# Kernel tuning notes

Measured on AMD Instinct MI355X. Metric: run time of the kernel, lower is better.

The kernel has to match this reference:

```python
import jax, jax.numpy as jnp
import numpy as np

N, E, L, F, HID, OUT = 20000, 200000, 5, 4, 128, 3


def _lin(x, w, b):
    # torch Linear convention: w is [out, in]
    return x @ w.T + b


def setup_inputs() -> dict:
    key = jax.random.key(0)
    ks = iter(jax.random.split(key, 40))
    nrm = lambda shape, s=0.05: jax.random.normal(next(ks), shape, dtype=jnp.float32) * s
    inp = {
        'x': jax.random.normal(next(ks), (N, L, F), dtype=jnp.float32),
        'edge_index': jax.random.randint(next(ks), (2, E), 0, N, dtype=jnp.int64),
        'edge_attr': jax.random.normal(next(ks), (E, F), dtype=jnp.float32),
        'batch': jnp.zeros((N,), dtype=jnp.int64),
        'node_type': jax.random.normal(next(ks), (N, 1), dtype=jnp.float32),
        # PastStateEncoder params
        'emb': nrm((L, F), 1.0),
        'conv_w': nrm((HID, 2 * F, 3)),  # Conv1d(8,128,3) OIW
        'conv_b': nrm((HID,)),
        # FusionLayer Linear(129,128)
        'fuse_w': nrm((HID, HID + 1)), 'fuse_b': nrm((HID,)),
        # gnn1 EdgeModel: Linear(2*128+4,128), Linear(128,128)
        'g1e_w1': nrm((HID, 2 * HID + F)), 'g1e_b1': nrm((HID,)),
        'g1e_w2': nrm((HID, HID)), 'g1e_b2': nrm((HID,)),
        # gnn1 NodeModel: Linear(256,128), Linear(128,128)
        'g1n_w1': nrm((HID, 2 * HID)), 'g1n_b1': nrm((HID,)),
        'g1n_w2': nrm((HID, HID)), 'g1n_b2': nrm((HID,)),
        # gnn2 EdgeModel: Linear(2*128+128,128), Linear(128,128)
        'g2e_w1': nrm((HID, 3 * HID)), 'g2e_b1': nrm((HID,)),
        'g2e_w2': nrm((HID, HID)), 'g2e_b2': nrm((HID,)),
        # gnn2 NodeModel
        'g2n_w1': nrm((HID, 2 * HID)), 'g2n_b1': nrm((HID,)),
        'g2n_w2': nrm((HID, HID)), 'g2n_b2': nrm((HID,)),
        # final_mlp: Linear(128,128), BN(128), Linear(128,3)
        'fm_w1': nrm((HID, HID)), 'fm_b1': nrm((HID,)),
        'bn_g': jnp.ones((HID,), dtype=jnp.float32), 'bn_b': jnp.zeros((HID,), dtype=jnp.float32),
        'fm_w2': nrm((OUT, HID)), 'fm_b2': nrm((OUT,)),
    }
    return inp


def _encoder(x, emb, conv_w, conv_b):
    # x: [N, L, F]; append learned positional embedding -> [N, L, 2F]
    n = x.shape[0]
    xe = jnp.concatenate([x, jnp.broadcast_to(emb[None], (n, L, F))], axis=-1)
    xc = xe.transpose(0, 2, 1)  # [N, 2F, L]
    y = jax.lax.conv_general_dilated(
        xc, conv_w, window_strides=(1,), padding=[(1, 1)],
        dimension_numbers=('NCW', 'OIW', 'NCW'))
    y = y + conv_b[None, :, None]
    return y.mean(axis=-1)  # [N, HID]


def _edge_mlp(src, dst, ea, w1, b1, w2, b2):
    h = jax.nn.relu(_lin(jnp.concatenate([src, dst, ea], axis=1), w1, b1))
    return _lin(h, w2, b2)


def _node_mlp(x_row, ea, w1, b1, w2, b2):
    h = jax.nn.relu(_lin(jnp.concatenate([x_row, ea], axis=1), w1, b1))
    return _lin(h, w2, b2)


def reference(x, edge_index, edge_attr, batch, node_type,
              emb, conv_w, conv_b, fuse_w, fuse_b,
              g1e_w1, g1e_b1, g1e_w2, g1e_b2, g1n_w1, g1n_b1, g1n_w2, g1n_b2,
              g2e_w1, g2e_b1, g2e_w2, g2e_b2, g2n_w1, g2n_b1, g2n_w2, g2n_b2,
              fm_w1, fm_b1, bn_g, bn_b, fm_w2, fm_b2):
    row, col = edge_index[0], edge_index[1]
    h = _encoder(x, emb, conv_w, conv_b)                     # [N,128]
    h = _lin(jnp.concatenate([h, node_type], axis=-1), fuse_w, fuse_b)  # [N,128]
    # gnn1 (MetaLayer: edge model then node model; node model here is per-edge)
    ea = _edge_mlp(h[row], h[col], edge_attr, g1e_w1, g1e_b1, g1e_w2, g1e_b2)  # [E,128]
    h = _node_mlp(h[row], ea, g1n_w1, g1n_b1, g1n_w2, g1n_b2)                  # [E,128]
    # gnn2 (h now lives on edges; indices < N <= E remain valid, matching torch)
    ea = _edge_mlp(h[row], h[col], ea, g2e_w1, g2e_b1, g2e_w2, g2e_b2)
    h = _node_mlp(h[row], ea, g2n_w1, g2n_b1, g2n_w2, g2n_b2)
    # final head on edge_attr: Linear -> BatchNorm1d (training stats) -> ReLU -> Linear
    z = _lin(ea, fm_w1, fm_b1)
    mu = z.mean(axis=0)
    var = z.var(axis=0)  # biased, matches torch BN normalization
    z = (z - mu) * jax.lax.rsqrt(var + 1e-5) * bn_g + bn_b
    z = jax.nn.relu(z)
    return _lin(z, fm_w2, fm_b2)  # [E,3]
```

## Files before the change

### kernel.cpp

```cpp
#include <hip/hip_runtime.h>

#define N_NODES 20000
#define N_EDGES 200000
#define HID 128
#define STR 136
#define NBLK 3125
#define NREP 64

typedef unsigned short u16;
using bf16x8 = __attribute__((ext_vector_type(8))) __bf16;
using f32x4  = __attribute__((ext_vector_type(4))) float;

__device__ __forceinline__ u16 f2bf(float f) {
  union { float f; unsigned u; } v; v.f = f;
  unsigned u = v.u;
  return (u16)((u + 0x7FFFu + ((u >> 16) & 1u)) >> 16);
}
__device__ __forceinline__ float bf2f(unsigned s) {
  union { unsigned u; float f; } v; v.u = s << 16;
  return v.f;
}
__device__ __forceinline__ bf16x8 ld8(const u16* p) { return *(const bf16x8*)p; }

__device__ __forceinline__ void zero_acc8(f32x4 acc[4]) {
#pragma unroll
  for (int i = 0; i < 4; ++i) acc[i] = (f32x4){0.f, 0.f, 0.f, 0.f};
}

template <int KSTEPS, typename AF>
__device__ __forceinline__ void wgemm8(const u16* __restrict__ PW, AF afrag,
                                       f32x4 acc[4], int lane, int wave) {
  const u16* pb = PW + (wave * 64 + lane) * 8;
  bf16x8 b[2];
  b[0] = ld8(pb);
#pragma unroll
  for (int ks = 0; ks < KSTEPS; ++ks) {
    const int cur = ks & 1;
    if (ks + 1 < KSTEPS) b[cur ^ 1] = ld8(pb + (ks + 1) * 4096);
#pragma unroll
    for (int mt = 0; mt < 4; ++mt) {
      bf16x8 a = afrag(ks, mt);
      acc[mt] = __builtin_amdgcn_mfma_f32_16x16x32_bf16(a, b[cur], acc[mt], 0, 0, 0);
    }
  }
}

template <bool RELU>
__device__ __forceinline__ void epi_store8(u16* buf, const f32x4 acc[4],
                                           const float* __restrict__ bias,
                                           int lane, int wave) {
  const int c = lane & 15, q = lane >> 4;
  const float bb = bias[wave * 16 + c];
  const int col = wave * 16 + c;
#pragma unroll
  for (int mt = 0; mt < 4; ++mt)
#pragma unroll
    for (int r = 0; r < 4; ++r) {
      float v = acc[mt][r] + bb;
      if (RELU) v = fmaxf(v, 0.f);
      buf[(mt * 16 + q * 4 + r) * STR + col] = f2bf(v);
    }
}

__device__ __forceinline__ void flush_buf8(const u16* buf, u16* __restrict__ gout,
                                           int e0, int tid) {
#pragma unroll
  for (int it = 0; it < 2; ++it) {
    int cid = tid + it * 512, e = cid >> 4, p = cid & 15;
    uint4 v = *(const uint4*)(buf + e * STR + p * 8);
    *(uint4*)(gout + (size_t)(e0 + e) * HID + p * 8) = v;
  }
}

__device__ __forceinline__ void stage_gather8(const int* __restrict__ rowI,
                                              const int* __restrict__ colI,
                                              const u16* __restrict__ htab,
                                              u16* B0, u16* B1,
                                              int e0, int lane, int wave) {
  const int r = lane >> 4, p = lane & 15;
#pragma unroll
  for (int it = 0; it < 4; ++it) {
    int j = wave * 16 + it * 4 + r;
    int e = j & 63;
    int id = (j < 64) ? rowI[e0 + e] : colI[e0 + e];
    uint4 v = *(const uint4*)(htab + (size_t)id * HID + p * 8);
    *(uint4*)(((j < 64) ? B0 : B1) + e * STR + p * 8) = v;
  }
}

__global__ __launch_bounds__(128) void k_prep1(
    const float* __restrict__ emb, const float* __restrict__ conv_w,
    const float* __restrict__ conv_b, const float* __restrict__ fuse_w,
    const float* __restrict__ fuse_b,
    const float* __restrict__ fm_w1, const float* __restrict__ g2e_b2,
    const float* __restrict__ fm_b1, const float* __restrict__ w6,
    float* __restrict__ Mt, float* __restrict__ C0, float* __restrict__ Wnt,
    float* __restrict__ b67, float* __restrict__ W67, float* __restrict__ bnrep) {
  __shared__ float red[22][129];
  __shared__ float w7s[128];
  const int o = blockIdx.x;
  const int j = threadIdx.x;
  bnrep[o * 128 + j] = 0.f;
  float A[21];
  {
    float b0 = conv_b[j];
#pragma unroll
    for (int p = 0; p < 5; ++p) {
#pragma unroll
      for (int i = 0; i < 8; ++i) {
        float s = 0.f;
#pragma unroll
        for (int k = 0; k < 3; ++k) {
          int t = p + 1 - k;
          if (t >= 0 && t < 5) s += conv_w[(j * 8 + i) * 3 + k];
        }
        s *= 0.2f;
        if (i < 4) A[p * 4 + i] = s;
        else b0 += emb[p * 4 + (i - 4)] * s;
      }
    }
    A[20] = b0;
  }
  float w = fuse_w[o * 129 + j];
  float w7 = fm_w1[o * 128 + j];
  w7s[j] = w7;
#pragma unroll
  for (int qq = 0; qq < 21; ++qq) red[qq][j] = w * A[qq];
  red[21][j] = w7 * g2e_b2[j];
  __syncthreads();
  if (j < 22) {
    float s = 0.f;
    for (int t = 0; t < 128; ++t) s += red[j][t];
    if (j < 20)      Mt[j * 128 + o] = s;
    else if (j == 20) C0[o] = s + fuse_b[o];
    else              b67[o] = s + fm_b1[o];
  }
  if (j == 0) Wnt[o] = fuse_w[o * 129 + 128];
  float s = 0.f;
  for (int t = 0; t < 128; ++t) s += w7s[t] * w6[t * 128 + j];
  W67[o * 128 + j] = s;
}

struct PackArgs {
  const float* src[6];
  u16* dst[6];
  int Kin[6];
  int ksCum[7];
};

__global__ __launch_bounds__(256) void k_prep2(
    PackArgs pa, const float* __restrict__ x, const float* __restrict__ node_type,
    const float* __restrict__ Mt, const float* __restrict__ C0,
    const float* __restrict__ Wnt, u16* __restrict__ h2) {
  if (blockIdx.x < 41) {
    int bk = blockIdx.x;
    int mi = 0;
    while (bk >= pa.ksCum[mi + 1]) ++mi;
    int ks = bk - pa.ksCum[mi];
    const float* W = pa.src[mi];
    u16* D = pa.dst[mi] + ks * 4096;
    int Kin = pa.Kin[mi];
#pragma unroll
    for (int t = 0; t < 16; ++t) {
      int el = t * 256 + (int)threadIdx.x;
      int j = el & 7, ln = (el >> 3) & 63, ntile = el >> 9;
      int k = ks * 32 + ((ln >> 4) << 3) + j;
      int n = ntile * 16 + (ln & 15);
      float v = (k < Kin) ? W[n * Kin + k] : 0.0f;
      D[el] = f2bf(v);
    }
    return;
  }
  __shared__ float xs[16][20], nts[16], mts[20 * 128];
  const int tid = threadIdx.x;
  const int n0 = ((int)blockIdx.x - 41) * 16;
  for (int i = tid; i < 320; i += 256) xs[i / 20][i % 20] = x[n0 * 20 + i];
  if (tid < 16) nts[tid] = node_type[n0 + tid];
  for (int i = tid; i < 2560; i += 256) mts[i] = Mt[i];
  __syncthreads();
  const int nl = tid >> 4;
  const int c0 = (tid & 15) * 8;
  float nt = nts[nl];
  union { u16 s[8]; uint4 u; } o;
#pragma unroll
  for (int i = 0; i < 8; ++i) {
    int ch = c0 + i;
    float acc = C0[ch] + Wnt[ch] * nt;
#pragma unroll
    for (int qq = 0; qq < 20; ++qq) acc += xs[nl][qq] * mts[qq * 128 + ch];
    o.s[i] = f2bf(acc);
  }
  *(uint4*)(h2 + (size_t)(n0 + nl) * HID + c0) = o.u;
}

__global__ __launch_bounds__(512, 8) void k_gnn1(
    const int* __restrict__ eidx, const float* __restrict__ eattr,
    const u16* __restrict__ h2, const u16* __restrict__ pW1, const u16* __restrict__ pW2,
    const u16* __restrict__ pW3, const u16* __restrict__ pW4, const float* __restrict__ b1,
    const float* __restrict__ b2, const float* __restrict__ b3, const float* __restrict__ b4,
    u16* __restrict__ ea1, u16* __restrict__ h3) {
  __shared__ __align__(16) u16 B0[64 * STR], B1[64 * STR];
  const int tid = threadIdx.x, lane = tid & 63, wave = tid >> 6;
  const int e0 = blockIdx.x * 64;
  const int m = lane & 15, q = lane >> 4;
  const int aoff = m * STR + q * 8;
  const int* rowI = eidx;
  const int* colI = eidx + N_EDGES;

  stage_gather8(rowI, colI, h2, B0, B1, e0, lane, wave);

  bf16x8 ef[4];
#pragma unroll
  for (int mt = 0; mt < 4; ++mt) {
    union { u16 s[8]; uint4 u; bf16x8 v; } t;
    t.u = make_uint4(0u, 0u, 0u, 0u);
    if (q == 0) {
      float4 a = *(const float4*)(eattr + (size_t)(e0 + mt * 16 + m) * 4);
      t.s[0] = f2bf(a.x); t.s[1] = f2bf(a.y); t.s[2] = f2bf(a.z); t.s[3] = f2bf(a.w);
    }
    ef[mt] = t.v;
  }
  __syncthreads();

  f32x4 acc[4];
  zero_acc8(acc);
  wgemm8<9>(pW1, [&](int ks, int mt) -> bf16x8 {
    if (ks < 4) return ld8(B0 + aoff + mt * 16 * STR + ks * 32);
    if (ks < 8) return ld8(B1 + aoff + mt * 16 * STR + (ks - 4) * 32);
    return ef[mt];
  }, acc, lane, wave);
  __syncthreads();
  epi_store8<true>(B1, acc, b1, lane, wave);
  __syncthreads();

  zero_acc8(acc);
  wgemm8<4>(pW2, [&](int ks, int mt) -> bf16x8 {
    return ld8(B1 + aoff + mt * 16 * STR + ks * 32);
  }, acc, lane, wave);
  epi_store8<false>(B0, acc, b2, lane, wave);
  __syncthreads();
  flush_buf8(B0, ea1, e0, tid);

  if (e0 < N_NODES) {
#pragma unroll
    for (int it = 0; it < 2; ++it) {
      int e = wave * 8 + it * 4 + q;
      int id = rowI[e0 + e];
      uint4 v = *(const uint4*)(h2 + (size_t)id * HID + m * 8);
      *(uint4*)(B1 + e * STR + m * 8) = v;
    }
    __syncthreads();

    zero_acc8(acc);
    wgemm8<8>(pW3, [&](int ks, int mt) -> bf16x8 {
      if (ks < 4) return ld8(B1 + aoff + mt * 16 * STR + ks * 32);
      return ld8(B0 + aoff + mt * 16 * STR + (ks - 4) * 32);
    }, acc, lane, wave);
    __syncthreads();
    epi_store8<true>(B1, acc, b3, lane, wave);
    __syncthreads();

    zero_acc8(acc);
    wgemm8<4>(pW4, [&](int ks, int mt) -> bf16x8 {
      return ld8(B1 + aoff + mt * 16 * STR + ks * 32);
    }, acc, lane, wave);
    epi_store8<false>(B0, acc, b4, lane, wave);
    __syncthreads();
    flush_buf8(B0, h3, e0, tid);
  }
}

__global__ __launch_bounds__(512, 8) void k_gnn2(
    const int* __restrict__ eidx, const u16* __restrict__ h3, u16* ea1z,
    const u16* __restrict__ pW5, const u16* __restrict__ pW67,
    const float* __restrict__ b5, const float* __restrict__ b67,
    float* __restrict__ bnrep) {
  __shared__ __align__(16) u16 B0[64 * STR], B1[64 * STR];
  const int tid = threadIdx.x, lane = tid & 63, wave = tid >> 6;
  const int e0 = blockIdx.x * 64;
  const int m = lane & 15, q = lane >> 4;
  const int aoff = m * STR + q * 8;
  const int* rowI = eidx;
  const int* colI = eidx + N_EDGES;

  stage_gather8(rowI, colI, h3, B0, B1, e0, lane, wave);
  __syncthreads();

  f32x4 acc[4];
  zero_acc8(acc);
  wgemm8<8>(pW5, [&](int ks, int mt) -> bf16x8 {
    if (ks < 4) return ld8(B0 + aoff + mt * 16 * STR + ks * 32);
    return ld8(B1 + aoff + mt * 16 * STR + (ks - 4) * 32);
  }, acc, lane, wave);
  __syncthreads();

#pragma unroll
  for (int it = 0; it < 2; ++it) {
    int cid = tid + it * 512, e = cid >> 4, p = cid & 15;
    uint4 v = *(const uint4*)(ea1z + (size_t)(e0 + e) * HID + p * 8);
    *(uint4*)(B0 + e * STR + p * 8) = v;
  }
  __syncthreads();

  wgemm8<4>(pW5 + 8 * 4096, [&](int ks, int mt) -> bf16x8 {
    return ld8(B0 + aoff + mt * 16 * STR + ks * 32);
  }, acc, lane, wave);
  epi_store8<true>(B1, acc, b5, lane, wave);
  __syncthreads();

  zero_acc8(acc);
  wgemm8<4>(pW67, [&](int ks, int mt) -> bf16x8 {
    return ld8(B1 + aoff + mt * 16 * STR + ks * 32);
  }, acc, lane, wave);

  {
    const int c = lane & 15;
    const int col = wave * 16 + c;
    const float bb = b67[col];
    float s0 = 0.f, q0 = 0.f;
#pragma unroll
    for (int mt = 0; mt < 4; ++mt)
#pragma unroll
      for (int r = 0; r < 4; ++r) {
        float v0 = acc[mt][r] + bb;
        s0 += v0; q0 += v0 * v0;
        int row = mt * 16 + q * 4 + r;
        B0[row * STR + col] = f2bf(v0);
      }
    s0 += __shfl_xor(s0, 16); s0 += __shfl_xor(s0, 32);
    q0 += __shfl_xor(q0, 16); q0 += __shfl_xor(q0, 32);
    if (lane < 16) {
      float* slot = bnrep + ((int)blockIdx.x & (NREP - 1)) * 256;
      atomicAdd(&slot[wave * 16 + lane], s0);
      atomicAdd(&slot[128 + wave * 16 + lane], q0);
    }
  }
  __syncthreads();
  flush_buf8(B0, ea1z, e0, tid);
}

__global__ __launch_bounds__(256) void k_head(const u16* __restrict__ z,
                                              const float* __restrict__ bnrep,
                                              const float* __restrict__ bn_g,
                                              const float* __restrict__ bn_b,
                                              const float* __restrict__ w2,
                                              const float* __restrict__ b2,
                                              float* __restrict__ out) {
  __shared__ float sh_s[128], sh_h[128], sh_w0[128], sh_w1[128], sh_w2[128];
  const int tid = threadIdx.x;
  {
    float s = 0.f;
    for (int r = 0; r < NREP; ++r) s += bnrep[r * 256 + tid];
    __shared__ float acc2[256];
    acc2[tid] = s;
    __syncthreads();
    if (tid < 128) {
      const float inv = 1.0f / (float)N_EDGES;
      float mu = acc2[tid] * inv;
      float var = acc2[128 + tid] * inv - mu * mu;
      float sc = bn_g[tid] * rsqrtf(var + 1e-5f);
      sh_s[tid] = sc;
      sh_h[tid] = bn_b[tid] - mu * sc;
      sh_w0[tid] = w2[tid];
      sh_w1[tid] = w2[128 + tid];
      sh_w2[tid] = w2[256 + tid];
    }
    __syncthreads();
  }
  const int lane = tid & 63, wave = tid >> 6;
  const int g = lane >> 4;
  const int p = lane & 15;
  const int c0 = p * 8;
  const float bb0 = b2[0], bb1 = b2[1], bb2 = b2[2];
#pragma unroll 4
  for (int it = 0; it < 16; ++it) {
    int e = (int)blockIdx.x * 256 + wave * 64 + it * 4 + g;
    if (e >= N_EDGES) break;
    uint4 v = *(const uint4*)(z + (size_t)e * HID + c0);
    unsigned wv[4] = {v.x, v.y, v.z, v.w};
    float a0 = 0.f, a1 = 0.f, a2 = 0.f;
#pragma unroll
    for (int k = 0; k < 4; ++k) {
      int ch = c0 + k * 2;
      float lo = bf2f(wv[k] & 0xffffu), hi = bf2f(wv[k] >> 16);
      float r0 = fmaxf(fmaf(lo, sh_s[ch], sh_h[ch]), 0.f);
      float r1 = fmaxf(fmaf(hi, sh_s[ch + 1], sh_h[ch + 1]), 0.f);
      a0 += r0 * sh_w0[ch] + r1 * sh_w0[ch + 1];
      a1 += r0 * sh_w1[ch] + r1 * sh_w1[ch + 1];
      a2 += r0 * sh_w2[ch] + r1 * sh_w2[ch + 1];
    }
#pragma unroll
    for (int off = 1; off < 16; off <<= 1) {
      a0 += __shfl_xor(a0, off);
      a1 += __shfl_xor(a1, off);
      a2 += __shfl_xor(a2, off);
    }
    if (p < 3) out[e * 3 + p] = (p == 0) ? a0 + bb0 : (p == 1) ? a1 + bb1 : a2 + bb2;
  }
}

extern "C" void kernel_launch(void* const* d_in, const int* in_sizes, int n_in,
                              void* d_out, int out_size, void* d_ws, size_t ws_size,
                              hipStream_t stream) {
  const float* x         = (const float*)d_in[0];
  const int* eidx        = (const int*)d_in[1];
  const float* eattr     = (const float*)d_in[2];
  const float* node_type = (const float*)d_in[4];
  const float* emb       = (const float*)d_in[5];
  const float* conv_w    = (const float*)d_in[6];
  const float* conv_b    = (const float*)d_in[7];
  const float* fuse_w    = (const float*)d_in[8];
  const float* fuse_b    = (const float*)d_in[9];
  const float* g1e_w1    = (const float*)d_in[10];
  const float* g1e_b1    = (const float*)d_in[11];
  const float* g1e_w2    = (const float*)d_in[12];
  const float* g1e_b2    = (const float*)d_in[13];
  const float* g1n_w1    = (const float*)d_in[14];
  const float* g1n_b1    = (const float*)d_in[15];
  const float* g1n_w2    = (const float*)d_in[16];
  const float* g1n_b2    = (const float*)d_in[17];
  const float* g2e_w1    = (const float*)d_in[18];
  const float* g2e_b1    = (const float*)d_in[19];
  const float* g2e_w2    = (const float*)d_in[20];
  const float* g2e_b2    = (const float*)d_in[21];
  const float* fm_w1     = (const float*)d_in[26];
  const float* fm_b1     = (const float*)d_in[27];
  const float* bn_g      = (const float*)d_in[28];
  const float* bn_b      = (const float*)d_in[29];
  const float* fm_w2     = (const float*)d_in[30];
  const float* fm_b2     = (const float*)d_in[31];
  float* out = (float*)d_out;

  char* ws = (char*)d_ws;
  size_t off = 0;
  auto take = [&](size_t bytes) {
    void* p = ws + off;
    off = (off + bytes + 255) & ~(size_t)255;
    return p;
  };
  u16* h2   = (u16*)take((size_t)N_NODES * HID * 2);
  u16* h3   = (u16*)take((size_t)20032 * HID * 2);
  u16* ea1z = (u16*)take((size_t)N_EDGES * HID * 2);
  float* Mt    = (float*)take(20 * 128 * 4);
  float* C0    = (float*)take(128 * 4);
  float* Wnt   = (float*)take(128 * 4);
  float* b67   = (float*)take(128 * 4);
  float* W67f  = (float*)take(128 * 128 * 4);
  float* bnrep = (float*)take((size_t)NREP * 256 * 4);
  u16* pW1  = (u16*)take(9 * 4096 * 2);
  u16* pW2  = (u16*)take(4 * 4096 * 2);
  u16* pW3  = (u16*)take(8 * 4096 * 2);
  u16* pW4  = (u16*)take(4 * 4096 * 2);
  u16* pW5  = (u16*)take(12 * 4096 * 2);
  u16* pW67 = (u16*)take(4 * 4096 * 2);

  k_prep1<<<128, 128, 0, stream>>>(emb, conv_w, conv_b, fuse_w, fuse_b,
                                   fm_w1, g2e_b2, fm_b1, g2e_w2,
                                   Mt, C0, Wnt, b67, W67f, bnrep);

  PackArgs pa;
  const float* srcs[6] = {g1e_w1, g1e_w2, g1n_w1, g1n_w2, g2e_w1, W67f};
  u16* dsts[6] = {pW1, pW2, pW3, pW4, pW5, pW67};
  int kins[6] = {260, 128, 256, 128, 384, 128};
  int kst[6] = {9, 4, 8, 4, 12, 4};
  int cum = 0;
  for (int i = 0; i < 6; ++i) {
    pa.src[i] = srcs[i]; pa.dst[i] = dsts[i]; pa.Kin[i] = kins[i];
    pa.ksCum[i] = cum; cum += kst[i];
  }
  pa.ksCum[6] = cum;

  k_prep2<<<41 + N_NODES / 16, 256, 0, stream>>>(pa, x, node_type, Mt, C0, Wnt, h2);
  k_gnn1<<<NBLK, 512, 0, stream>>>(eidx, eattr, h2, pW1, pW2, pW3, pW4,
                                   g1e_b1, g1e_b2, g1n_b1, g1n_b2, ea1z, h3);
  k_gnn2<<<NBLK, 512, 0, stream>>>(eidx, h3, ea1z, pW5, pW67,
                                   g2e_b1, b67, bnrep);
  k_head<<<(N_EDGES + 255) / 256, 256, 0, stream>>>(ea1z, bnrep, bn_g, bn_b,
                                                    fm_w2, fm_b2, out);
}
```

Baseline: 232.4 us.

## Fuse all stages into one cooperative persistent kernel with grid syncs

Replaces the five separate launches with a single cooperative kernel that runs prep, encode, two GNN stages and the head, separated by grid-wide syncs. Edge tiles are claimed dynamically through an atomic counter in a persistent loop. The goal is to remove launch gaps and tail effects between kernels. The cost is grid.sync overhead, lower occupancy (512 blocks, launch bounds of 4 per CU), and atomic contention on the tile counter. A multi-kernel fallback runs if the cooperative launch fails.

```diff
diff --git a/kernel.cpp b/kernel.cpp
--- a/kernel.cpp
+++ b/kernel.cpp
@@ -1,4 +1,7 @@
 #include <hip/hip_runtime.h>
+#include <hip/hip_cooperative_groups.h>
+
+namespace cg = cooperative_groups;
 
 #define N_NODES 20000
 #define N_EDGES 200000
@@ -88,207 +91,213 @@
   }
 }
 
-__global__ __launch_bounds__(128) void k_prep1(
-    const float* __restrict__ emb, const float* __restrict__ conv_w,
-    const float* __restrict__ conv_b, const float* __restrict__ fuse_w,
-    const float* __restrict__ fuse_b,
-    const float* __restrict__ fm_w1, const float* __restrict__ g2e_b2,
-    const float* __restrict__ fm_b1, const float* __restrict__ w6,
-    float* __restrict__ Mt, float* __restrict__ C0, float* __restrict__ Wnt,
-    float* __restrict__ b67, float* __restrict__ W67, float* __restrict__ bnrep) {
-  __shared__ float red[22][129];
-  __shared__ float w7s[128];
-  const int o = blockIdx.x;
-  const int j = threadIdx.x;
-  bnrep[o * 128 + j] = 0.f;
-  float A[21];
-  {
-    float b0 = conv_b[j];
-#pragma unroll
-    for (int p = 0; p < 5; ++p) {
-#pragma unroll
-      for (int i = 0; i < 8; ++i) {
-        float s = 0.f;
-#pragma unroll
-        for (int k = 0; k < 3; ++k) {
-          int t = p + 1 - k;
-          if (t >= 0 && t < 5) s += conv_w[(j * 8 + i) * 3 + k];
+struct FusedArgs {
+  const float *x, *eattr, *node_type, *emb, *conv_w, *conv_b, *fuse_w, *fuse_b;
+  const float *g1e_b1, *g1e_b2, *g1n_b1, *g1n_b2, *g2e_b1, *g2e_b2;
+  const float *fm_w1, *fm_b1, *bn_g, *bn_b, *fm_w2, *fm_b2, *w6;
+  const int* eidx;
+  float* out;
+  u16 *h2, *h3, *ea1z, *pW1, *pW2, *pW3, *pW4, *pW5, *pW67;
+  float *Mt, *C0, *Wnt, *b67, *W67f, *bnrep;
+  int* ctr;
+  const float* psrc[6];
+  u16* pdst[6];
+  int pKin[6];
+  int pCum[7];
+};
+
+
+__device__ __forceinline__ void phase_prep1(const FusedArgs& fa, int bid, int gdim,
+                                            int tid, u16* SM) {
+  float* red = (float*)SM;
+  float* w7s = red + 22 * 129;
+  for (int o = bid; o < 128; o += gdim) {
+    __syncthreads();
+    if (tid < 128) {
+      const int j = tid;
+      float A[21];
+      {
+        float b0 = fa.conv_b[j];
+#pragma unroll
+        for (int p = 0; p < 5; ++p) {
+#pragma unroll
+          for (int i = 0; i < 8; ++i) {
+            float s = 0.f;
+#pragma unroll
+            for (int k = 0; k < 3; ++k) {
+              int tt = p + 1 - k;
+              if (tt >= 0 && tt < 5) s += fa.conv_w[(j * 8 + i) * 3 + k];
+            }
+            s *= 0.2f;
+            if (i < 4) A[p * 4 + i] = s;
+            else b0 += fa.emb[p * 4 + (i - 4)] * s;
+          }
         }
-        s *= 0.2f;
-        if (i < 4) A[p * 4 + i] = s;
-        else b0 += emb[p * 4 + (i - 4)] * s;
+        A[20] = b0;
       }
-    }
-    A[20] = b0;
-  }
-  float w = fuse_w[o * 129 + j];
-  float w7 = fm_w1[o * 128 + j];
-  w7s[j] = w7;
-#pragma unroll
-  for (int qq = 0; qq < 21; ++qq) red[qq][j] = w * A[qq];
-  red[21][j] = w7 * g2e_b2[j];
-  __syncthreads();
-  if (j < 22) {
-    float s = 0.f;
-    for (int t = 0; t < 128; ++t) s += red[j][t];
-    if (j < 20)      Mt[j * 128 + o] = s;
-    else if (j == 20) C0[o] = s + fuse_b[o];
-    else              b67[o] = s + fm_b1[o];
-  }
-  if (j == 0) Wnt[o] = fuse_w[o * 129 + 128];
-  float s = 0.f;
-  for (int t = 0; t < 128; ++t) s += w7s[t] * w6[t * 128 + j];
-  W67[o * 128 + j] = s;
-}
-
-struct PackArgs {
-  const float* src[6];
-  u16* dst[6];
-  int Kin[6];
-  int ksCum[7];
-};
-
-__global__ __launch_bounds__(256) void k_prep2(
-    PackArgs pa, const float* __restrict__ x, const float* __restrict__ node_type,
-    const float* __restrict__ Mt, const float* __restrict__ C0,
-    const float* __restrict__ Wnt, u16* __restrict__ h2) {
-  if (blockIdx.x < 41) {
-    int bk = blockIdx.x;
+      float w = fa.fuse_w[o * 129 + j];
+      float w7 = fa.fm_w1[o * 128 + j];
+      w7s[j] = w7;
+#pragma unroll
+      for (int qq = 0; qq < 21; ++qq) red[qq * 129 + j] = w * A[qq];
+      red[21 * 129 + j] = w7 * fa.g2e_b2[j];
+    }
+    __syncthreads();
+    if (tid < 22) {
+      float s = 0.f;
+      for (int u = 0; u < 128; ++u) s += red[tid * 129 + u];
+      if (tid < 20)       fa.Mt[tid * 128 + o] = s;
+      else if (tid == 20) fa.C0[o] = s + fa.fuse_b[o];
+      else                fa.b67[o] = s + fa.fm_b1[o];
+    }
+    if (tid == 0) fa.Wnt[o] = fa.fuse_w[o * 129 + 128];
+    if (tid < 128) {
+      float s = 0.f;
+      for (int u = 0; u < 128; ++u) s += w7s[u] * fa.w6[u * 128 + tid];
+      fa.W67f[o * 128 + tid] = s;
+    }
+  }
+}
+
+__device__ __forceinline__ void phase_zero(const FusedArgs& fa, int bid, int gdim,
+                                           int tid) {
+  for (int i = bid * 512 + tid; i < NREP * 256; i += gdim * 512) fa.bnrep[i] = 0.f;
+  if (bid == 0 && tid < 4) fa.ctr[tid] = 0;
+}
+
+__device__ __forceinline__ void phase_pack(const FusedArgs& fa, int bid, int gdim,
+                                           int tid) {
+  for (int b = bid; b < 41; b += gdim) {
     int mi = 0;
-    while (bk >= pa.ksCum[mi + 1]) ++mi;
-    int ks = bk - pa.ksCum[mi];
-    const float* W = pa.src[mi];
-    u16* D = pa.dst[mi] + ks * 4096;
-    int Kin = pa.Kin[mi];
-#pragma unroll
-    for (int t = 0; t < 16; ++t) {
-      int el = t * 256 + (int)threadIdx.x;
+    while (b >= fa.pCum[mi + 1]) ++mi;
+    int ks = b - fa.pCum[mi];
+    const float* W = fa.psrc[mi];
+    u16* D = fa.pdst[mi] + ks * 4096;
+    int Kin = fa.pKin[mi];
+#pragma unroll
+    for (int t = 0; t < 8; ++t) {
+      int el = t * 512 + tid;
       int j = el & 7, ln = (el >> 3) & 63, ntile = el >> 9;
       int k = ks * 32 + ((ln >> 4) << 3) + j;
       int n = ntile * 16 + (ln & 15);
       float v = (k < Kin) ? W[n * Kin + k] : 0.0f;
       D[el] = f2bf(v);
     }
-    return;
-  }
-  __shared__ float xs[16][20], nts[16], mts[20 * 128];
-  const int tid = threadIdx.x;
-  const int n0 = ((int)blockIdx.x - 41) * 16;
-  for (int i = tid; i < 320; i += 256) xs[i / 20][i % 20] = x[n0 * 20 + i];
-  if (tid < 16) nts[tid] = node_type[n0 + tid];
-  for (int i = tid; i < 2560; i += 256) mts[i] = Mt[i];
-  __syncthreads();
-  const int nl = tid >> 4;
-  const int c0 = (tid & 15) * 8;
-  float nt = nts[nl];
-  union { u16 s[8]; uint4 u; } o;
-#pragma unroll
-  for (int i = 0; i < 8; ++i) {
-    int ch = c0 + i;
-    float acc = C0[ch] + Wnt[ch] * nt;
-#pragma unroll
-    for (int qq = 0; qq < 20; ++qq) acc += xs[nl][qq] * mts[qq * 128 + ch];
-    o.s[i] = f2bf(acc);
-  }
-  *(uint4*)(h2 + (size_t)(n0 + nl) * HID + c0) = o.u;
-}
-
-__global__ __launch_bounds__(512, 8) void k_gnn1(
-    const int* __restrict__ eidx, const float* __restrict__ eattr,
-    const u16* __restrict__ h2, const u16* __restrict__ pW1, const u16* __restrict__ pW2,
-    const u16* __restrict__ pW3, const u16* __restrict__ pW4, const float* __restrict__ b1,
-    const float* __restrict__ b2, const float* __restrict__ b3, const float* __restrict__ b4,
-    u16* __restrict__ ea1, u16* __restrict__ h3) {
-  __shared__ __align__(16) u16 B0[64 * STR], B1[64 * STR];
-  const int tid = threadIdx.x, lane = tid & 63, wave = tid >> 6;
-  const int e0 = blockIdx.x * 64;
+  }
+}
+
+__device__ __forceinline__ void phase_encode(const FusedArgs& fa, int bid, int gdim,
+                                             int tid, u16* SM) {
+  float* xs  = (float*)SM;
+  float* nts = xs + 640;
+  float* mts = nts + 32;
+  for (int i = tid; i < 2560; i += 512) mts[i] = fa.Mt[i];
+  for (int c = bid; c < 625; c += gdim) {
+    __syncthreads();
+    for (int i = tid; i < 640; i += 512) xs[i] = fa.x[(size_t)c * 640 + i];
+    if (tid < 32) nts[tid] = fa.node_type[c * 32 + tid];
+    __syncthreads();
+    const int nl = tid >> 4;
+    const int c0 = (tid & 15) * 8;
+    float nt = nts[nl];
+    union { u16 s[8]; uint4 u; } o;
+#pragma unroll
+    for (int i = 0; i < 8; ++i) {
+      int ch = c0 + i;
+      float acc = fa.C0[ch] + fa.Wnt[ch] * nt;
+#pragma unroll
+      for (int qq = 0; qq < 20; ++qq) acc += xs[nl * 20 + qq] * mts[qq * 128 + ch];
+      o.s[i] = f2bf(acc);
+    }
+    *(uint4*)(fa.h2 + (size_t)(c * 32 + nl) * HID + c0) = o.u;
+  }
+}
+
+__device__ __forceinline__ void gnn1_tile(const FusedArgs& fa, u16* B0, u16* B1,
+                                          int t, int tid, int lane, int wave) {
+  const int e0 = t * 64;
   const int m = lane & 15, q = lane >> 4;
   const int aoff = m * STR + q * 8;
-  const int* rowI = eidx;
-  const int* colI = eidx + N_EDGES;
-
-  stage_gather8(rowI, colI, h2, B0, B1, e0, lane, wave);
+  const int* rowI = fa.eidx;
+  const int* colI = fa.eidx + N_EDGES;
+
+  stage_gather8(rowI, colI, fa.h2, B0, B1, e0, lane, wave);
 
   bf16x8 ef[4];
 #pragma unroll
   for (int mt = 0; mt < 4; ++mt) {
-    union { u16 s[8]; uint4 u; bf16x8 v; } t;
-    t.u = make_uint4(0u, 0u, 0u, 0u);
+    union { u16 s[8]; uint4 u; bf16x8 v; } tt;
+    tt.u = make_uint4(0u, 0u, 0u, 0u);
     if (q == 0) {
-      float4 a = *(const float4*)(eattr + (size_t)(e0 + mt * 16 + m) * 4);
-      t.s[0] = f2bf(a.x); t.s[1] = f2bf(a.y); t.s[2] = f2bf(a.z); t.s[3] = f2bf(a.w);
-    }
-    ef[mt] = t.v;
+      float4 a = *(const float4*)(fa.eattr + (size_t)(e0 + mt * 16 + m) * 4);
+      tt.s[0] = f2bf(a.x); tt.s[1] = f2bf(a.y); tt.s[2] = f2bf(a.z); tt.s[3] = f2bf(a.w);
+    }
+    ef[mt] = tt.v;
   }
   __syncthreads();
 
   f32x4 acc[4];
   zero_acc8(acc);
-  wgemm8<9>(pW1, [&](int ks, int mt) -> bf16x8 {
+  wgemm8<9>(fa.pW1, [&](int ks, int mt) -> bf16x8 {
     if (ks < 4) return ld8(B0 + aoff + mt * 16 * STR + ks * 32);
     if (ks < 8) return ld8(B1 + aoff + mt * 16 * STR + (ks - 4) * 32);
     return ef[mt];
   }, acc, lane, wave);
   __syncthreads();
-  epi_store8<true>(B1, acc, b1, lane, wave);
+  epi_store8<true>(B1, acc, fa.g1e_b1, lane, wave);
   __syncthreads();
 
   zero_acc8(acc);
-  wgemm8<4>(pW2, [&](int ks, int mt) -> bf16x8 {
+  wgemm8<4>(fa.pW2, [&](int ks, int mt) -> bf16x8 {
     return ld8(B1 + aoff + mt * 16 * STR + ks * 32);
   }, acc, lane, wave);
-  epi_store8<false>(B0, acc, b2, lane, wave);
-  __syncthreads();
-  flush_buf8(B0, ea1, e0, tid);
+  epi_store8<false>(B0, acc, fa.g1e_b2, lane, wave);
+  __syncthreads();
+  flush_buf8(B0, fa.ea1z, e0, tid);
 
   if (e0 < N_NODES) {
 #pragma unroll
     for (int it = 0; it < 2; ++it) {
-      int e = wave * 8 + it * 4 + q;
+      int cid = tid + it * 512, e = cid >> 4, p = cid & 15;
       int id = rowI[e0 + e];
-      uint4 v = *(const uint4*)(h2 + (size_t)id * HID + m * 8);
-      *(uint4*)(B1 + e * STR + m * 8) = v;
+      uint4 v = *(const uint4*)(fa.h2 + (size_t)id * HID + p * 8);
+      *(uint4*)(B1 + e * STR + p * 8) = v;
     }
     __syncthreads();
 
     zero_acc8(acc);
-    wgemm8<8>(pW3, [&](int ks, int mt) -> bf16x8 {
+    wgemm8<8>(fa.pW3, [&](int ks, int mt) -> bf16x8 {
       if (ks < 4) return ld8(B1 + aoff + mt * 16 * STR + ks * 32);
       return ld8(B0 + aoff + mt * 16 * STR + (ks - 4) * 32);
     }, acc, lane, wave);
     __syncthreads();
-    epi_store8<true>(B1, acc, b3, lane, wave);
+    epi_store8<true>(B1, acc, fa.g1n_b1, lane, wave);
     __syncthreads();
 
     zero_acc8(acc);
-    wgemm8<4>(pW4, [&](int ks, int mt) -> bf16x8 {
+    wgemm8<4>(fa.pW4, [&](int ks, int mt) -> bf16x8 {
       return ld8(B1 + aoff + mt * 16 * STR + ks * 32);
     }, acc, lane, wave);
-    epi_store8<false>(B0, acc, b4, lane, wave);
-    __syncthreads();
-    flush_buf8(B0, h3, e0, tid);
-  }
-}
-
-__global__ __launch_bounds__(512, 8) void k_gnn2(
-    const int* __restrict__ eidx, const u16* __restrict__ h3, u16* ea1z,
-    const u16* __restrict__ pW5, const u16* __restrict__ pW67,
-    const float* __restrict__ b5, const float* __restrict__ b67,
-    float* __restrict__ bnrep) {
-  __shared__ __align__(16) u16 B0[64 * STR], B1[64 * STR];
-  const int tid = threadIdx.x, lane = tid & 63, wave = tid >> 6;
-  const int e0 = blockIdx.x * 64;
+    epi_store8<false>(B0, acc, fa.g1n_b2, lane, wave);
+    __syncthreads();
+    flush_buf8(B0, fa.h3, e0, tid);
+  }
+}
+
+__device__ __forceinline__ void gnn2_tile(const FusedArgs& fa, u16* B0, u16* B1,
+                                          int t, int tid, int lane, int wave) {
+  const int e0 = t * 64;
   const int m = lane & 15, q = lane >> 4;
   const int aoff = m * STR + q * 8;
-  const int* rowI = eidx;
-  const int* colI = eidx + N_EDGES;
-
-  stage_gather8(rowI, colI, h3, B0, B1, e0, lane, wave);
+  const int* rowI = fa.eidx;
+  const int* colI = fa.eidx + N_EDGES;
+
+  stage_gather8(rowI, colI, fa.h3, B0, B1, e0, lane, wave);
   __syncthreads();
 
   f32x4 acc[4];
   zero_acc8(acc);
-  wgemm8<8>(pW5, [&](int ks, int mt) -> bf16x8 {
+  wgemm8<8>(fa.pW5, [&](int ks, int mt) -> bf16x8 {
     if (ks < 4) return ld8(B0 + aoff + mt * 16 * STR + ks * 32);
     return ld8(B1 + aoff + mt * 16 * STR + (ks - 4) * 32);
   }, acc, lane, wave);
@@ -297,26 +306,26 @@
 #pragma unroll
   for (int it = 0; it < 2; ++it) {
     int cid = tid + it * 512, e = cid >> 4, p = cid & 15;
-    uint4 v = *(const uint4*)(ea1z + (size_t)(e0 + e) * HID + p * 8);
+    uint4 v = *(const uint4*)(fa.ea1z + (size_t)(e0 + e) * HID + p * 8);
     *(uint4*)(B0 + e * STR + p * 8) = v;
   }
   __syncthreads();
 
-  wgemm8<4>(pW5 + 8 * 4096, [&](int ks, int mt) -> bf16x8 {
+  wgemm8<4>(fa.pW5 + 8 * 4096, [&](int ks, int mt) -> bf16x8 {
     return ld8(B0 + aoff + mt * 16 * STR + ks * 32);
   }, acc, lane, wave);
-  epi_store8<true>(B1, acc, b5, lane, wave);
+  epi_store8<true>(B1, acc, fa.g2e_b1, lane, wave);
   __syncthreads();
 
   zero_acc8(acc);
-  wgemm8<4>(pW67, [&](int ks, int mt) -> bf16x8 {
+  wgemm8<4>(fa.pW67, [&](int ks, int mt) -> bf16x8 {
     return ld8(B1 + aoff + mt * 16 * STR + ks * 32);
   }, acc, lane, wave);
 
   {
     const int c = lane & 15;
     const int col = wave * 16 + c;
-    const float bb = b67[col];
+    const float bb = fa.b67[col];
     float s0 = 0.f, q0 = 0.f;
 #pragma unroll
     for (int mt = 0; mt < 4; ++mt)
@@ -330,106 +339,170 @@
     s0 += __shfl_xor(s0, 16); s0 += __shfl_xor(s0, 32);
     q0 += __shfl_xor(q0, 16); q0 += __shfl_xor(q0, 32);
     if (lane < 16) {
-      float* slot = bnrep + ((int)blockIdx.x & (NREP - 1)) * 256;
+      float* slot = fa.bnrep + (t & (NREP - 1)) * 256;
       atomicAdd(&slot[wave * 16 + lane], s0);
       atomicAdd(&slot[128 + wave * 16 + lane], q0);
     }
   }
   __syncthreads();
-  flush_buf8(B0, ea1z, e0, tid);
-}
-
-__global__ __launch_bounds__(256) void k_head(const u16* __restrict__ z,
-                                              const float* __restrict__ bnrep,
-                                              const float* __restrict__ bn_g,
-                                              const float* __restrict__ bn_b,
-                                              const float* __restrict__ w2,
-                                              const float* __restrict__ b2,
-                                              float* __restrict__ out) {
-  __shared__ float sh_s[128], sh_h[128], sh_w0[128], sh_w1[128], sh_w2[128];
-  const int tid = threadIdx.x;
-  {
+  flush_buf8(B0, fa.ea1z, e0, tid);
+}
+
+__device__ __forceinline__ void phase_head(const FusedArgs& fa, int bid, int gdim,
+                                           int tid, u16* SM) {
+  float* fs = (float*)SM;
+  float* sh_s = fs;
+  float* sh_h = fs + 128;
+  float* sh_w0 = fs + 256;
+  float* sh_w1 = fs + 384;
+  float* sh_w2 = fs + 512;
+  float* acc2 = fs + 640;
+  __syncthreads();
+  if (tid < 256) {
     float s = 0.f;
-    for (int r = 0; r < NREP; ++r) s += bnrep[r * 256 + tid];
-    __shared__ float acc2[256];
+    for (int r = 0; r < NREP; ++r) s += fa.bnrep[r * 256 + tid];
     acc2[tid] = s;
-    __syncthreads();
-    if (tid < 128) {
-      const float inv = 1.0f / (float)N_EDGES;
-      float mu = acc2[tid] * inv;
-      float var = acc2[128 + tid] * inv - mu * mu;
-      float sc = bn_g[tid] * rsqrtf(var + 1e-5f);
-      sh_s[tid] = sc;
-      sh_h[tid] = bn_b[tid] - mu * sc;
-      sh_w0[tid] = w2[tid];
-      sh_w1[tid] = w2[128 + tid];
-      sh_w2[tid] = w2[256 + tid];
-    }
-    __syncthreads();
-  }
+  }
+  __syncthreads();
+  if (tid < 128) {
+    const float inv = 1.0f / (float)N_EDGES;
+    float mu = acc2[tid] * inv;
+    float var = acc2[128 + tid] * inv - mu * mu;
+    float sc = fa.bn_g[tid] * rsqrtf(var + 1e-5f);
+    sh_s[tid] = sc;
+    sh_h[tid] = fa.bn_b[tid] - mu * sc;
+    sh_w0[tid] = fa.fm_w2[tid];
+    sh_w1[tid] = fa.fm_w2[128 + tid];
+    sh_w2[tid] = fa.fm_w2[256 + tid];
+  }
+  __syncthreads();
   const int lane = tid & 63, wave = tid >> 6;
   const int g = lane >> 4;
   const int p = lane & 15;
   const int c0 = p * 8;
-  const float bb0 = b2[0], bb1 = b2[1], bb2 = b2[2];
+  const float bb0 = fa.fm_b2[0], bb1 = fa.fm_b2[1], bb2 = fa.fm_b2[2];
+  for (int b = bid; b < (N_EDGES + 511) / 512; b += gdim) {
 #pragma unroll 4
-  for (int it = 0; it < 16; ++it) {
-    int e = (int)blockIdx.x * 256 + wave * 64 + it * 4 + g;
-    if (e >= N_EDGES) break;
-    uint4 v = *(const uint4*)(z + (size_t)e * HID + c0);
-    unsigned wv[4] = {v.x, v.y, v.z, v.w};
-    float a0 = 0.f, a1 = 0.f, a2 = 0.f;
-#pragma unroll
-    for (int k = 0; k < 4; ++k) {
-      int ch = c0 + k * 2;
-      float lo = bf2f(wv[k] & 0xffffu), hi = bf2f(wv[k] >> 16);
-      float r0 = fmaxf(fmaf(lo, sh_s[ch], sh_h[ch]), 0.f);
-      float r1 = fmaxf(fmaf(hi, sh_s[ch + 1], sh_h[ch + 1]), 0.f);
-      a0 += r0 * sh_w0[ch] + r1 * sh_w0[ch + 1];
-      a1 += r0 * sh_w1[ch] + r1 * sh_w1[ch + 1];
-      a2 += r0 * sh_w2[ch] + r1 * sh_w2[ch + 1];
-    }
-#pragma unroll
-    for (int off = 1; off < 16; off <<= 1) {
-      a0 += __shfl_xor(a0, off);
-      a1 += __shfl_xor(a1, off);
-      a2 += __shfl_xor(a2, off);
-    }
-    if (p < 3) out[e * 3 + p] = (p == 0) ? a0 + bb0 : (p == 1) ? a1 + bb1 : a2 + bb2;
-  }
+    for (int it = 0; it < 16; ++it) {
+      int e = b * 512 + wave * 64 + it * 4 + g;
+      if (e >= N_EDGES) break;
+      uint4 v = *(const uint4*)(fa.ea1z + (size_t)e * HID + c0);
+      unsigned wv[4] = {v.x, v.y, v.z, v.w};
+      float a0 = 0.f, a1 = 0.f, a2 = 0.f;
+#pragma unroll
+      for (int k = 0; k < 4; ++k) {
+        int ch = c0 + k * 2;
+        float lo = bf2f(wv[k] & 0xffffu), hi = bf2f(wv[k] >> 16);
+        float r0 = fmaxf(fmaf(lo, sh_s[ch], sh_h[ch]), 0.f);
+        float r1 = fmaxf(fmaf(hi, sh_s[ch + 1], sh_h[ch + 1]), 0.f);
+        a0 += r0 * sh_w0[ch] + r1 * sh_w0[ch + 1];
+        a1 += r0 * sh_w1[ch] + r1 * sh_w1[ch + 1];
+        a2 += r0 * sh_w2[ch] + r1 * sh_w2[ch + 1];
+      }
+#pragma unroll
+      for (int off = 1; off < 16; off <<= 1) {
+        a0 += __shfl_xor(a0, off);
+        a1 += __shfl_xor(a1, off);
+        a2 += __shfl_xor(a2, off);
+      }
+      if (p < 3) fa.out[e * 3 + p] = (p == 0) ? a0 + bb0 : (p == 1) ? a1 + bb1 : a2 + bb2;
+    }
+  }
+}
+
+__global__ __launch_bounds__(512, 4) void k_fused(FusedArgs fa) {
+  cg::grid_group grid = cg::this_grid();
+  __shared__ __align__(16) u16 SM[64 * STR * 2];
+  __shared__ int tsh;
+  u16* B0 = SM;
+  u16* B1 = SM + 64 * STR;
+  const int tid = threadIdx.x, lane = tid & 63, wave = tid >> 6;
+  const int bid = (int)blockIdx.x, gdim = (int)gridDim.x;
+
+  phase_prep1(fa, bid, gdim, tid, SM);
+  phase_zero(fa, bid, gdim, tid);
+  grid.sync();
+  phase_pack(fa, bid, gdim, tid);
+  phase_encode(fa, bid, gdim, tid, SM);
+  grid.sync();
+  for (;;) {
+    __syncthreads();
+    if (tid == 0) tsh = atomicAdd(&fa.ctr[0], 1);
+    __syncthreads();
+    int t = tsh;
+    if (t >= NBLK) break;
+    gnn1_tile(fa, B0, B1, t, tid, lane, wave);
+  }
+  grid.sync();
+  for (;;) {
+    __syncthreads();
+    if (tid == 0) tsh = atomicAdd(&fa.ctr[1], 1);
+    __syncthreads();
+    int t = tsh;
+    if (t >= NBLK) break;
+    gnn2_tile(fa, B0, B1, t, tid, lane, wave);
+  }
+  grid.sync();
+  phase_head(fa, bid, gdim, tid, SM);
+}
+
+__global__ __launch_bounds__(512) void k_s0(FusedArgs fa) {
+  __shared__ __align__(16) u16 SM[64 * STR * 2];
+  phase_prep1(fa, blockIdx.x, gridDim.x, threadIdx.x, SM);
+  phase_zero(fa, blockIdx.x, gridDim.x, threadIdx.x);
+}
+__global__ __launch_bounds__(512) void k_s1(FusedArgs fa) {
+  __shared__ __align__(16) u16 SM[64 * STR * 2];
+  phase_pack(fa, blockIdx.x, gridDim.x, threadIdx.x);
+  phase_encode(fa, blockIdx.x, gridDim.x, threadIdx.x, SM);
+}
+__global__ __launch_bounds__(512, 4) void k_s2(FusedArgs fa) {
+  __shared__ __align__(16) u16 SM[64 * STR * 2];
+  const int tid = threadIdx.x;
+  gnn1_tile(fa, SM, SM + 64 * STR, blockIdx.x, tid, tid & 63, tid >> 6);
+}
+__global__ __launch_bounds__(512, 4) void k_s3(FusedArgs fa) {
+  __shared__ __align__(16) u16 SM[64 * STR * 2];
+  const int tid = threadIdx.x;
+  gnn2_tile(fa, SM, SM + 64 * STR, blockIdx.x, tid, tid & 63, tid >> 6);
+}
+__global__ __launch_bounds__(512) void k_s4(FusedArgs fa) {
+  __shared__ __align__(16) u16 SM[64 * STR * 2];
+  phase_head(fa, blockIdx.x, gridDim.x, threadIdx.x, SM);
 }
 
 extern "C" void kernel_launch(void* const* d_in, const int* in_sizes, int n_in,
                               void* d_out, int out_size, void* d_ws, size_t ws_size,
                               hipStream_t stream) {
-  const float* x         = (const float*)d_in[0];
-  const int* eidx        = (const int*)d_in[1];
-  const float* eattr     = (const float*)d_in[2];
-  const float* node_type = (const float*)d_in[4];
-  const float* emb       = (const float*)d_in[5];
-  const float* conv_w    = (const float*)d_in[6];
-  const float* conv_b    = (const float*)d_in[7];
-  const float* fuse_w    = (const float*)d_in[8];
-  const float* fuse_b    = (const float*)d_in[9];
-  const float* g1e_w1    = (const float*)d_in[10];
-  const float* g1e_b1    = (const float*)d_in[11];
-  const float* g1e_w2    = (const float*)d_in[12];
-  const float* g1e_b2    = (const float*)d_in[13];
-  const float* g1n_w1    = (const float*)d_in[14];
-  const float* g1n_b1    = (const float*)d_in[15];
-  const float* g1n_w2    = (const float*)d_in[16];
-  const float* g1n_b2    = (const float*)d_in[17];
-  const float* g2e_w1    = (const float*)d_in[18];
-  const float* g2e_b1    = (const float*)d_in[19];
-  const float* g2e_w2    = (const float*)d_in[20];
-  const float* g2e_b2    = (const float*)d_in[21];
-  const float* fm_w1     = (const float*)d_in[26];
-  const float* fm_b1     = (const float*)d_in[27];
-  const float* bn_g      = (const float*)d_in[28];
-  const float* bn_b      = (const float*)d_in[29];
-  const float* fm_w2     = (const float*)d_in[30];
-  const float* fm_b2     = (const float*)d_in[31];
-  float* out = (float*)d_out;
+  FusedArgs fa;
+  fa.x         = (const float*)d_in[0];
+  fa.eidx      = (const int*)d_in[1];
+  fa.eattr     = (const float*)d_in[2];
+  fa.node_type = (const float*)d_in[4];
+  fa.emb       = (const float*)d_in[5];
+  fa.conv_w    = (const float*)d_in[6];
+  fa.conv_b    = (const float*)d_in[7];
+  fa.fuse_w    = (const float*)d_in[8];
+  fa.fuse_b    = (const float*)d_in[9];
+  const float* g1e_w1 = (const float*)d_in[10];
+  fa.g1e_b1    = (const float*)d_in[11];
+  const float* g1e_w2 = (const float*)d_in[12];
+  fa.g1e_b2    = (const float*)d_in[13];
+  const float* g1n_w1 = (const float*)d_in[14];
+  fa.g1n_b1    = (const float*)d_in[15];
+  const float* g1n_w2 = (const float*)d_in[16];
+  fa.g1n_b2    = (const float*)d_in[17];
+  const float* g2e_w1 = (const float*)d_in[18];
+  fa.g2e_b1    = (const float*)d_in[19];
+  fa.w6        = (const float*)d_in[20];
+  fa.g2e_b2    = (const float*)d_in[21];
+  fa.fm_w1     = (const float*)d_in[26];
+  fa.fm_b1     = (const float*)d_in[27];
+  fa.bn_g      = (const float*)d_in[28];
+  fa.bn_b      = (const float*)d_in[29];
+  fa.fm_w2     = (const float*)d_in[30];
+  fa.fm_b2     = (const float*)d_in[31];
+  fa.out = (float*)d_out;
 
   char* ws = (char*)d_ws;
   size_t off = 0;
@@ -438,43 +511,45 @@
     off = (off + bytes + 255) & ~(size_t)255;
     return p;
   };
-  u16* h2   = (u16*)take((size_t)N_NODES * HID * 2);
-  u16* h3   = (u16*)take((size_t)20032 * HID * 2);
-  u16* ea1z = (u16*)take((size_t)N_EDGES * HID * 2);
-  float* Mt    = (float*)take(20 * 128 * 4);
-  float* C0    = (float*)take(128 * 4);
-  float* Wnt   = (float*)take(128 * 4);
-  float* b67   = (float*)take(128 * 4);
-  float* W67f  = (float*)take(128 * 128 * 4);
-  float* bnrep = (float*)take((size_t)NREP * 256 * 4);
-  u16* pW1  = (u16*)take(9 * 4096 * 2);
-  u16* pW2  = (u16*)take(4 * 4096 * 2);
-  u16* pW3  = (u16*)take(8 * 4096 * 2);
-  u16* pW4  = (u16*)take(4 * 4096 * 2);
-  u16* pW5  = (u16*)take(12 * 4096 * 2);
-  u16* pW67 = (u16*)take(4 * 4096 * 2);
-
-  k_prep1<<<128, 128, 0, stream>>>(emb, conv_w, conv_b, fuse_w, fuse_b,
-                                   fm_w1, g2e_b2, fm_b1, g2e_w2,
-                                   Mt, C0, Wnt, b67, W67f, bnrep);
-
-  PackArgs pa;
-  const float* srcs[6] = {g1e_w1, g1e_w2, g1n_w1, g1n_w2, g2e_w1, W67f};
-  u16* dsts[6] = {pW1, pW2, pW3, pW4, pW5, pW67};
+  fa.h2   = (u16*)take((size_t)N_NODES * HID * 2);
+  fa.h3   = (u16*)take((size_t)20032 * HID * 2);
+  fa.ea1z = (u16*)take((size_t)N_EDGES * HID * 2);
+  fa.Mt    = (float*)take(20 * 128 * 4);
+  fa.C0    = (float*)take(128 * 4);
+  fa.Wnt   = (float*)take(128 * 4);
+  fa.b67   = (float*)take(128 * 4);
+  fa.W67f  = (float*)take(128 * 128 * 4);
+  fa.bnrep = (float*)take((size_t)NREP * 256 * 4);
+  fa.pW1  = (u16*)take(9 * 4096 * 2);
+  fa.pW2  = (u16*)take(4 * 4096 * 2);
+  fa.pW3  = (u16*)take(8 * 4096 * 2);
+  fa.pW4  = (u16*)take(4 * 4096 * 2);
+  fa.pW5  = (u16*)take(12 * 4096 * 2);
+  fa.pW67 = (u16*)take(4 * 4096 * 2);
+  fa.ctr  = (int*)take(4 * 4);
+
+  const float* srcs[6] = {g1e_w1, g1e_w2, g1n_w1, g1n_w2, g2e_w1, fa.W67f};
+  u16* dsts[6] = {fa.pW1, fa.pW2, fa.pW3, fa.pW4, fa.pW5, fa.pW67};
   int kins[6] = {260, 128, 256, 128, 384, 128};
   int kst[6] = {9, 4, 8, 4, 12, 4};
   int cum = 0;
   for (int i = 0; i < 6; ++i) {
-    pa.src[i] = srcs[i]; pa.dst[i] = dsts[i]; pa.Kin[i] = kins[i];
-    pa.ksCum[i] = cum; cum += kst[i];
-  }
-  pa.ksCum[6] = cum;
-
-  k_prep2<<<41 + N_NODES / 16, 256, 0, stream>>>(pa, x, node_type, Mt, C0, Wnt, h2);
-  k_gnn1<<<NBLK, 512, 0, stream>>>(eidx, eattr, h2, pW1, pW2, pW3, pW4,
-                                   g1e_b1, g1e_b2, g1n_b1, g1n_b2, ea1z, h3);
-  k_gnn2<<<NBLK, 512, 0, stream>>>(eidx, h3, ea1z, pW5, pW67,
-                                   g2e_b1, b67, bnrep);
-  k_head<<<(N_EDGES + 255) / 256, 256, 0, stream>>>(ea1z, bnrep, bn_g, bn_b,
-                                                    fm_w2, fm_b2, out);
-}
+    fa.psrc[i] = srcs[i]; fa.pdst[i] = dsts[i]; fa.pKin[i] = kins[i];
+    fa.pCum[i] = cum; cum += kst[i];
+  }
+  fa.pCum[6] = cum;
+
+  void* params[] = {(void*)&fa};
+  hipError_t err = hipLaunchCooperativeKernel((const void*)k_fused, dim3(512),
+                                              dim3(512), params, 0, stream);
+  if (err != hipSuccess)
+    err = hipLaunchCooperativeKernel((const void*)k_fused, dim3(256),
+                                     dim3(512), params, 0, stream);
+  if (err != hipSuccess) {
+    k_s0<<<256, 512, 0, stream>>>(fa);
+    k_s1<<<666, 512, 0, stream>>>(fa);
+    k_s2<<<NBLK, 512, 0, stream>>>(fa);
+    k_s3<<<NBLK, 512, 0, stream>>>(fa);
+    k_s4<<<391, 512, 0, stream>>>(fa);
+  }
+}
```

Result: slower. 528.9 us (+127.6%).
